# Performance work log

Hardware: AMD Instinct MI355X
Metric: run time of the kernel (lower is better)

The kernel has to match this reference:

```python
import jax, jax.numpy as jnp
import numpy as np

N = 100000   # nodes
E = 1600000  # edges
F_IN = 128
H = 128
C = 40


def setup_inputs() -> dict:
    key = jax.random.key(0)
    ks = jax.random.split(key, 8)
    s = 0.05
    return {
        "x": jax.random.normal(ks[0], (N, F_IN), dtype=jnp.float32),
        "edge_index": jax.random.randint(ks[1], (2, E), 0, N, dtype=jnp.int32),
        "W1": jax.random.normal(ks[2], (F_IN, H), dtype=jnp.float32) * s,
        "b1": jnp.zeros((H,), jnp.float32),
        "W2": jax.random.normal(ks[3], (H, H), dtype=jnp.float32) * s,
        "b2": jnp.zeros((H,), jnp.float32),
        "Wfc": jax.random.normal(ks[4], (H, C), dtype=jnp.float32) * s,
        "bfc": jnp.zeros((C,), jnp.float32),
    }


def _graph_conv(x, src, dst, norm_out, norm_in, W, b):
    # DGL GraphConv, norm='both': h = D_in^{-1/2} A D_out^{-1/2} x W + b
    h = (x * norm_out[:, None]) @ W                      # [N, H] (W first: in>=out)
    agg = jax.ops.segment_sum(h[src], dst, num_segments=N)  # gather + scatter-add
    return agg * norm_in[:, None] + b


def reference(x, edge_index, W1, b1, W2, b2, Wfc, bfc):
    src, dst = edge_index[0], edge_index[1]
    ones = jnp.ones((E,), x.dtype)
    deg_out = jnp.maximum(jax.ops.segment_sum(ones, src, num_segments=N), 1.0)
    deg_in = jnp.maximum(jax.ops.segment_sum(ones, dst, num_segments=N), 1.0)
    norm_out = jax.lax.rsqrt(deg_out)
    norm_in = jax.lax.rsqrt(deg_in)
    # layer 0: GraphConv + relu (dropout is identity in eval mode)
    h = jax.nn.relu(_graph_conv(x, src, dst, norm_out, norm_in, W1, b1))
    # layer 1: GraphConv, no activation
    h = _graph_conv(h, src, dst, norm_out, norm_in, W2, b2)
    # final FC
    return h @ Wfc + bfc
```

## Files before the change

kernel.cpp:

```cpp
#include <hip/hip_runtime.h>
#include <hip/hip_fp16.h>


#define CHUNK    4096
#define NBK      800
#define SLAB     3072

typedef __attribute__((ext_vector_type(8))) short bf16x8;
typedef __attribute__((ext_vector_type(4))) float f32x4;

struct __align__(8)  half4 { __half x, y, z, w; };
struct __align__(16) half8 { __half h[8]; };

__device__ __forceinline__ unsigned short f2bf(float f) {
    union { float f; unsigned u; } v; v.f = f;
    unsigned r = v.u + 0x7FFFu + ((v.u >> 16) & 1u);
    return (unsigned short)(r >> 16);
}
__device__ __forceinline__ float bf2f(unsigned short h) {
    union { unsigned u; float f; } v; v.u = ((unsigned)h) << 16;
    return v.f;
}

__global__ void setup_kernel(const float* __restrict__ W1, const float* __restrict__ W2,
                             const float* __restrict__ Wfc,
                             const float* __restrict__ b2, const float* __restrict__ bfc,
                             unsigned short* __restrict__ Wh1, unsigned short* __restrict__ Wl1,
                             unsigned short* __restrict__ Wh2, unsigned short* __restrict__ Wl2,
                             float* __restrict__ b2p,
                             int* __restrict__ cur_d, int* __restrict__ cur_s, int nbuck) {
    int idx = blockIdx.x * blockDim.x + threadIdx.x;
    if (idx < nbuck) { cur_d[idx] = idx * SLAB; cur_s[idx] = idx * SLAB; }

    if (idx < 16384) {
        int k = idx >> 7, nn = idx & 127;
        float v = W1[idx];
        int q = k >> 5, j = k & 7, lb = ((k >> 3) & 3) * 16;
        int tcol = nn >> 4;
        int l = lb + (nn & 15);
        int pos = ((tcol * 4 + q) * 64 + l) * 8 + j;
        unsigned short h = f2bf(v);
        Wh1[pos] = h;
        Wl1[pos] = f2bf(v - bf2f(h));
    } else if (idx < 16384 + 6144) {
        int i2 = idx - 16384;
        int k = i2 / 48, nn = i2 - k * 48;
        float v = 0.f;
        if (nn < 40) {
            const float* w2row = W2 + k * 128;
            #pragma unroll 8
            for (int jj = 0; jj < 128; ++jj) v += w2row[jj] * Wfc[jj * 40 + nn];
        }
        int t = nn >> 4, q = k >> 5, j = k & 7;
        int l = ((k >> 3) & 3) * 16 + (nn & 15);
        int pos = ((t * 4 + q) * 64 + l) * 8 + j;
        unsigned short h = f2bf(v);
        Wh2[pos] = h;
        Wl2[pos] = f2bf(v - bf2f(h));
    } else if (idx < 16384 + 6144 + 40) {
        int c = idx - (16384 + 6144);
        float a = bfc[c];
        #pragma unroll 8
        for (int j = 0; j < 128; ++j) a += b2[j] * Wfc[j * 40 + c];
        b2p[c] = a;
    }
}

__global__ __launch_bounds__(256) void scatter_res_kernel(
        const int* __restrict__ src, const int* __restrict__ dst,
        int* __restrict__ cur_d, int* __restrict__ cur_s,
        unsigned int* __restrict__ ppack, unsigned char* __restrict__ es_loc,
        int E) {
    __shared__ int hd[NBK], hs[NBK], bd[NBK], bs[NBK];
    const int tid = threadIdx.x;
    for (int i = tid; i < NBK; i += 256) { hd[i] = 0; hs[i] = 0; }
    __syncthreads();
    const int base = blockIdx.x * CHUNK;
    const int end  = min(base + CHUNK, E);
    for (int e = base + tid; e < end; e += 256) {
        atomicAdd(&hd[((unsigned)dst[e]) >> 7], 1);
        atomicAdd(&hs[((unsigned)src[e]) >> 7], 1);
    }
    __syncthreads();
    for (int i = tid; i < NBK; i += 256) {
        int cd = hd[i];
        bd[i] = cd ? atomicAdd(&cur_d[i], cd) : 0;
        hd[i] = 0;
        int cs = hs[i];
        bs[i] = cs ? atomicAdd(&cur_s[i], cs) : 0;
        hs[i] = 0;
    }
    __syncthreads();
    for (int e = base + tid; e < end; e += 256) {
        int d = dst[e], s = src[e];
        unsigned bin_d = ((unsigned)d) >> 7;
        int pos = bd[bin_d] + atomicAdd(&hd[bin_d], 1);
        ppack[pos] = (((unsigned)d & 127u) << 17) | (unsigned)s;
        unsigned bin_s = ((unsigned)s) >> 7;
        int ps = bs[bin_s] + atomicAdd(&hs[bin_s], 1);
        es_loc[ps] = (unsigned char)(s & 127);
    }
}

__global__ __launch_bounds__(256) void fine_kernel(
        const unsigned int* __restrict__ ppack, const int* __restrict__ cur_d,
        const unsigned char* __restrict__ es_loc, const int* __restrict__ cur_s,
        int* __restrict__ deg_in, float* __restrict__ norm_in,
        int* __restrict__ row_ptr, int* __restrict__ csr_src,
        float* __restrict__ norm_out, int N_) {
    __shared__ int h[128];
    __shared__ int psum[128];
    const int tid = threadIdx.x;
    const int b = blockIdx.x;
    const int start = b * SLAB;
    const int node  = (b << 7) + tid;

    const int end_d = cur_d[b];
    if (tid < 128) h[tid] = 0;
    __syncthreads();
    for (int i = start + tid; i < end_d; i += 256)
        atomicAdd(&h[ppack[i] >> 17], 1);
    __syncthreads();

    int a = 0;
    if (tid < 128) { a = h[tid]; psum[tid] = a; }
    __syncthreads();
    for (int off = 1; off < 128; off <<= 1) {
        int t = 0;
        if (tid < 128 && tid >= off) t = psum[tid - off];
        __syncthreads();
        if (tid < 128) psum[tid] += t;
        __syncthreads();
    }

    if (tid < 128) {
        int base0 = psum[tid] - a + start;
        if (node < N_) {
            deg_in[node]  = a;
            row_ptr[node] = base0;
            norm_in[node] = rsqrtf((float)(a < 1 ? 1 : a));
        }
        h[tid] = base0;
    }
    __syncthreads();

    for (int i = start + tid; i < end_d; i += 256) {
        unsigned int pk = ppack[i];
        int pos = atomicAdd(&h[pk >> 17], 1);
        csr_src[pos] = (int)(pk & 0x1FFFFu);
    }
    __syncthreads();

    const int end_s = cur_s[b];
    if (tid < 128) h[tid] = 0;
    __syncthreads();
    for (int i = start + tid; i < end_s; i += 256)
        atomicAdd(&h[(int)es_loc[i]], 1);
    __syncthreads();

    if (tid < 128 && node < N_) {
        int d = h[tid];
        norm_out[node] = rsqrtf((float)(d < 1 ? 1 : d));
    }
}

__global__ __launch_bounds__(256, 3) void gemm128(
        const float* __restrict__ X, const float* __restrict__ scale,
        const unsigned short* __restrict__ Wh, const unsigned short* __restrict__ Wl,
        __half* __restrict__ Y, int nrows) {
    const int tid  = threadIdx.x;
    const int lane = tid & 63;
    const int w    = tid >> 6;
    const int m    = lane & 15;
    const int quad = lane >> 4;
    const int rowBase = blockIdx.x * 128 + w * 32;

    bf16x8 Ah[2][4], Al[2][4];
    #pragma unroll
    for (int rt = 0; rt < 2; ++rt) {
        int r = rowBase + rt * 16 + m;
        float sc = (r < nrows) ? scale[r] : 0.f;
        const float* xr = X + (size_t)(r < nrows ? r : 0) * 128;
        #pragma unroll
        for (int q = 0; q < 4; ++q) {
            int k0 = q * 32 + quad * 8;
            float4 a = *(const float4*)(xr + k0);
            float4 bv = *(const float4*)(xr + k0 + 4);
            float v[8] = {a.x * sc, a.y * sc, a.z * sc, a.w * sc,
                          bv.x * sc, bv.y * sc, bv.z * sc, bv.w * sc};
            bf16x8 hi, lo;
            #pragma unroll
            for (int j = 0; j < 8; ++j) {
                unsigned short h = f2bf(v[j]);
                hi[j] = (short)h;
                lo[j] = (short)f2bf(v[j] - bf2f(h));
            }
            Ah[rt][q] = hi; Al[rt][q] = lo;
        }
    }

    f32x4 acc[2][8];
    #pragma unroll
    for (int rt = 0; rt < 2; ++rt)
        #pragma unroll
        for (int t = 0; t < 8; ++t)
            acc[rt][t] = (f32x4){0.f, 0.f, 0.f, 0.f};

    #pragma unroll
    for (int t = 0; t < 8; ++t) {
        #pragma unroll
        for (int q = 0; q < 4; ++q) {
            const int off = ((t * 4 + q) * 64 + lane) * 8;
            bf16x8 Bh = *(const bf16x8*)(Wh + off);
            bf16x8 Bl = *(const bf16x8*)(Wl + off);
            #pragma unroll
            for (int rt = 0; rt < 2; ++rt) {
                acc[rt][t] = __builtin_amdgcn_mfma_f32_16x16x32_bf16(Ah[rt][q], Bh, acc[rt][t], 0, 0, 0);
                acc[rt][t] = __builtin_amdgcn_mfma_f32_16x16x32_bf16(Ah[rt][q], Bl, acc[rt][t], 0, 0, 0);
                acc[rt][t] = __builtin_amdgcn_mfma_f32_16x16x32_bf16(Al[rt][q], Bh, acc[rt][t], 0, 0, 0);
            }
        }
    }

    #pragma unroll
    for (int rt = 0; rt < 2; ++rt) {
        int r0 = rowBase + rt * 16 + quad * 4;
        #pragma unroll
        for (int reg = 0; reg < 4; ++reg) {
            int r = r0 + reg;
            if (r >= nrows) continue;
            __half* yr = Y + (size_t)r * 128 + m;
            #pragma unroll
            for (int t = 0; t < 8; ++t)
                yr[t * 16] = __float2half(acc[rt][t][reg]);
        }
    }
}

__global__ __launch_bounds__(256, 4) void gather_kernel(
        const __half* __restrict__ H, const int* __restrict__ row_ptr,
        const int* __restrict__ deg, const int* __restrict__ csr_src,
        const float* __restrict__ norm_in, const float* __restrict__ b,
        const float* __restrict__ norm_out,
        const unsigned short* __restrict__ Wh2, const unsigned short* __restrict__ Wl2,
        __half* __restrict__ G, int n) {
    __shared__ unsigned short h1h[16][136];
    __shared__ unsigned short h1l[16][136];
    const int tid   = threadIdx.x;
    const int node0 = blockIdx.x * 16;
    const int g     = tid >> 4;
    const int node  = node0 + g;
    const int c     = (tid & 15) * 8;
    const bool active = node < n;

    int start = 0, cnt = 0;
    if (active) { start = row_ptr[node]; cnt = deg[node]; }
    float acc[8] = {0.f, 0.f, 0.f, 0.f, 0.f, 0.f, 0.f, 0.f};

    int j = 0;
    for (; j + 4 <= cnt; j += 4) {
        int s0 = csr_src[start + j];
        int s1 = csr_src[start + j + 1];
        int s2 = csr_src[start + j + 2];
        int s3 = csr_src[start + j + 3];
        half8 v0 = *(const half8*)(H + (long long)s0 * 128 + c);
        half8 v1 = *(const half8*)(H + (long long)s1 * 128 + c);
        half8 v2 = *(const half8*)(H + (long long)s2 * 128 + c);
        half8 v3 = *(const half8*)(H + (long long)s3 * 128 + c);
        #pragma unroll
        for (int k = 0; k < 8; ++k)
            acc[k] += (__half2float(v0.h[k]) + __half2float(v1.h[k]))
                    + (__half2float(v2.h[k]) + __half2float(v3.h[k]));
    }
    for (; j < cnt; ++j) {
        int s0 = csr_src[start + j];
        half8 v0 = *(const half8*)(H + (long long)s0 * 128 + c);
        #pragma unroll
        for (int k = 0; k < 8; ++k) acc[k] += __half2float(v0.h[k]);
    }

    float ni = active ? norm_in[node]  : 0.f;
    float no = active ? norm_out[node] : 0.f;
    float4 b0  = *(const float4*)(b + c);
    float4 b1v = *(const float4*)(b + c + 4);
    float bb[8] = {b0.x, b0.y, b0.z, b0.w, b1v.x, b1v.y, b1v.z, b1v.w};
    bf16x8 hi, lo;
    #pragma unroll
    for (int k = 0; k < 8; ++k) {
        float hv = fmaxf(acc[k] * ni + bb[k], 0.f) * no;
        unsigned short h = f2bf(hv);
        hi[k] = (short)h;
        lo[k] = (short)f2bf(hv - bf2f(h));
    }
    *(bf16x8*)&h1h[g][c] = hi;
    *(bf16x8*)&h1l[g][c] = lo;
    __syncthreads();

    const int w = tid >> 6;
    if (w < 3) {
        const int lane = tid & 63;
        const int m    = lane & 15;
        const int quad = lane >> 4;

        f32x4 a3 = (f32x4){0.f, 0.f, 0.f, 0.f};
        const int t = w;
        #pragma unroll
        for (int q = 0; q < 4; ++q) {
            const int k0 = q * 32 + quad * 8;
            bf16x8 Ah = *(const bf16x8*)&h1h[m][k0];
            bf16x8 Al = *(const bf16x8*)&h1l[m][k0];
            const int off = ((t * 4 + q) * 64 + lane) * 8;
            bf16x8 Bh = *(const bf16x8*)(Wh2 + off);
            bf16x8 Bl = *(const bf16x8*)(Wl2 + off);
            a3 = __builtin_amdgcn_mfma_f32_16x16x32_bf16(Ah, Bh, a3, 0, 0, 0);
            a3 = __builtin_amdgcn_mfma_f32_16x16x32_bf16(Ah, Bl, a3, 0, 0, 0);
            a3 = __builtin_amdgcn_mfma_f32_16x16x32_bf16(Al, Bh, a3, 0, 0, 0);
        }

        const int col = t * 16 + m;
        if (col < 40) {
            const int r0 = node0 + quad * 4;
            #pragma unroll
            for (int reg = 0; reg < 4; ++reg) {
                int r = r0 + reg;
                if (r < n) G[(size_t)r * 64 + col] = __float2half(a3[reg]);
            }
        }
    }
}

__global__ __launch_bounds__(256) void gather40_kernel(
        const __half* __restrict__ G, const int* __restrict__ row_ptr,
        const int* __restrict__ deg, const int* __restrict__ csr_src,
        const float* __restrict__ norm_in, const float* __restrict__ b2p,
        float* __restrict__ out, int n) {
    const int t = blockIdx.x * 256 + threadIdx.x;
    if (t >= n * 5) return;
    const int node = t / 5;
    const int c    = (t - node * 5) * 8;

    const int start = row_ptr[node];
    const int cnt   = deg[node];
    float acc[8] = {0.f, 0.f, 0.f, 0.f, 0.f, 0.f, 0.f, 0.f};

    int j = 0;
    for (; j + 4 <= cnt; j += 4) {
        int s0 = csr_src[start + j];
        int s1 = csr_src[start + j + 1];
        int s2 = csr_src[start + j + 2];
        int s3 = csr_src[start + j + 3];
        half8 v0 = *(const half8*)(G + (long long)s0 * 64 + c);
        half8 v1 = *(const half8*)(G + (long long)s1 * 64 + c);
        half8 v2 = *(const half8*)(G + (long long)s2 * 64 + c);
        half8 v3 = *(const half8*)(G + (long long)s3 * 64 + c);
        #pragma unroll
        for (int k = 0; k < 8; ++k)
            acc[k] += (__half2float(v0.h[k]) + __half2float(v1.h[k]))
                    + (__half2float(v2.h[k]) + __half2float(v3.h[k]));
    }
    for (; j < cnt; ++j) {
        int s0 = csr_src[start + j];
        half8 v0 = *(const half8*)(G + (long long)s0 * 64 + c);
        #pragma unroll
        for (int k = 0; k < 8; ++k) acc[k] += __half2float(v0.h[k]);
    }

    float ni = norm_in[node];
    float4 o0, o1;
    o0.x = acc[0] * ni + b2p[c + 0];
    o0.y = acc[1] * ni + b2p[c + 1];
    o0.z = acc[2] * ni + b2p[c + 2];
    o0.w = acc[3] * ni + b2p[c + 3];
    o1.x = acc[4] * ni + b2p[c + 4];
    o1.y = acc[5] * ni + b2p[c + 5];
    o1.z = acc[6] * ni + b2p[c + 6];
    o1.w = acc[7] * ni + b2p[c + 7];
    float* op = out + (long long)node * 40 + c;
    *(float4*)(op)     = o0;
    *(float4*)(op + 4) = o1;
}

extern "C" void kernel_launch(void* const* d_in, const int* in_sizes, int n_in,
                              void* d_out, int out_size, void* d_ws, size_t ws_size,
                              hipStream_t stream) {
    const float* x   = (const float*)d_in[0];
    const int*   ei  = (const int*)  d_in[1];
    const float* W1  = (const float*)d_in[2];
    const float* b1  = (const float*)d_in[3];
    const float* W2  = (const float*)d_in[4];
    const float* b2  = (const float*)d_in[5];
    const float* Wfc = (const float*)d_in[6];
    const float* bfc = (const float*)d_in[7];
    float* out = (float*)d_out;

    const int N = in_sizes[0] / 128;
    const int E = in_sizes[1] / 2;
    const int* src = ei;
    const int* dst = ei + E;

    const int nbuck = (N + 127) >> 7;
    const int B1 = (E + CHUNK - 1) / CHUNK;

    char* p = (char*)d_ws;
    float* norm_out = (float*)p; p += (size_t)N * 4;
    float* norm_in  = (float*)p; p += (size_t)N * 4;
    float* bufA     = (float*)p; p += (size_t)N * 128 * 4;
    float* bufB     = (float*)p; p += (size_t)N * 128 * 4;
    int*   deg_in   = (int*)p;   p += (size_t)N * 4;
    int*   row_ptr  = (int*)p;   p += (size_t)N * 4;
    int*   csr_src  = (int*)p;   p += (size_t)NBK * SLAB * 4;
    int*   cur_d    = (int*)p;   p += (size_t)1024 * 4;
    int*   cur_s    = (int*)p;   p += (size_t)1024 * 4;
    float* b2p      = (float*)p; p += (size_t)64 * 4;
    unsigned short* Wh1 = (unsigned short*)p; p += (size_t)16384 * 2;
    unsigned short* Wl1 = (unsigned short*)p; p += (size_t)16384 * 2;
    unsigned short* Wh2 = (unsigned short*)p; p += (size_t)6144 * 2;
    unsigned short* Wl2 = (unsigned short*)p; p += (size_t)6144 * 2;

    unsigned int*  ppack  = (unsigned int*)bufB;
    unsigned char* es_loc = (unsigned char*)(ppack + (size_t)NBK * SLAB);

    __half* h1pre = (__half*)bufA;
    __half* G     = (__half*)bufB;

    const int T = 256;

    setup_kernel<<<(16384 + 6144 + 40 + T - 1) / T, T, 0, stream>>>(
        W1, W2, Wfc, b2, bfc, Wh1, Wl1, Wh2, Wl2, b2p, cur_d, cur_s, nbuck);
    scatter_res_kernel<<<B1, T, 0, stream>>>(src, dst, cur_d, cur_s, ppack, es_loc, E);
    fine_kernel<<<nbuck, T, 0, stream>>>(ppack, cur_d, es_loc, cur_s,
                                         deg_in, norm_in, row_ptr, csr_src,
                                         norm_out, N);

    const int gemm_grid = (N + 127) / 128;
    gemm128<<<gemm_grid, T, 0, stream>>>(x, norm_out, Wh1, Wl1, h1pre, N);
    const int gather_grid = (N + 15) / 16;
    gather_kernel<<<gather_grid, T, 0, stream>>>(h1pre, row_ptr, deg_in, csr_src,
                                                 norm_in, b1, norm_out,
                                                 Wh2, Wl2, G, N);
    gather40_kernel<<<((size_t)N * 5 + T - 1) / T, T, 0, stream>>>(
        G, row_ptr, deg_in, csr_src, norm_in, b2p, out, N);
}
```

Before: 277.5 us.

## Fuse edge scatter with layer-1 GEMM and move norm_out into gather

The layer-1 GEMM no longer scales rows by norm_out, so it no longer depends on the degree computation. It is merged into the edge-scatter launch as extra blocks, letting the two independent stages run at the same time and removing one kernel launch. To make up for it, the gather kernel loads norm_out for every source edge and multiplies it in with fma. This adds 1.6M scattered 4-byte reads in exchange for the overlap, and the fused kernel now shares LDS and register limits between two very different workloads.

New measurement: 276.6 us. No clear change (-0.3%).

```diff
diff --git a/kernel.cpp b/kernel.cpp
--- a/kernel.cpp
+++ b/kernel.cpp
@@ -66,39 +66,114 @@
     }
 }
 
-__global__ __launch_bounds__(256) void scatter_res_kernel(
+__global__ __launch_bounds__(256, 3) void fat_kernel(
         const int* __restrict__ src, const int* __restrict__ dst,
         int* __restrict__ cur_d, int* __restrict__ cur_s,
         unsigned int* __restrict__ ppack, unsigned char* __restrict__ es_loc,
-        int E) {
+        int E, int nsc,
+        const float* __restrict__ X,
+        const unsigned short* __restrict__ Wh, const unsigned short* __restrict__ Wl,
+        __half* __restrict__ Y, int nrows) {
     __shared__ int hd[NBK], hs[NBK], bd[NBK], bs[NBK];
     const int tid = threadIdx.x;
-    for (int i = tid; i < NBK; i += 256) { hd[i] = 0; hs[i] = 0; }
-    __syncthreads();
-    const int base = blockIdx.x * CHUNK;
-    const int end  = min(base + CHUNK, E);
-    for (int e = base + tid; e < end; e += 256) {
-        atomicAdd(&hd[((unsigned)dst[e]) >> 7], 1);
-        atomicAdd(&hs[((unsigned)src[e]) >> 7], 1);
-    }
-    __syncthreads();
-    for (int i = tid; i < NBK; i += 256) {
-        int cd = hd[i];
-        bd[i] = cd ? atomicAdd(&cur_d[i], cd) : 0;
-        hd[i] = 0;
-        int cs = hs[i];
-        bs[i] = cs ? atomicAdd(&cur_s[i], cs) : 0;
-        hs[i] = 0;
-    }
-    __syncthreads();
-    for (int e = base + tid; e < end; e += 256) {
-        int d = dst[e], s = src[e];
-        unsigned bin_d = ((unsigned)d) >> 7;
-        int pos = bd[bin_d] + atomicAdd(&hd[bin_d], 1);
-        ppack[pos] = (((unsigned)d & 127u) << 17) | (unsigned)s;
-        unsigned bin_s = ((unsigned)s) >> 7;
-        int ps = bs[bin_s] + atomicAdd(&hs[bin_s], 1);
-        es_loc[ps] = (unsigned char)(s & 127);
+
+    if (blockIdx.x < nsc) {
+        for (int i = tid; i < NBK; i += 256) { hd[i] = 0; hs[i] = 0; }
+        __syncthreads();
+        const int base = blockIdx.x * CHUNK;
+        const int end  = min(base + CHUNK, E);
+        for (int e = base + tid; e < end; e += 256) {
+            atomicAdd(&hd[((unsigned)dst[e]) >> 7], 1);
+            atomicAdd(&hs[((unsigned)src[e]) >> 7], 1);
+        }
+        __syncthreads();
+        for (int i = tid; i < NBK; i += 256) {
+            int cd = hd[i];
+            bd[i] = cd ? atomicAdd(&cur_d[i], cd) : 0;
+            hd[i] = 0;
+            int cs = hs[i];
+            bs[i] = cs ? atomicAdd(&cur_s[i], cs) : 0;
+            hs[i] = 0;
+        }
+        __syncthreads();
+        for (int e = base + tid; e < end; e += 256) {
+            int d = dst[e], s = src[e];
+            unsigned bin_d = ((unsigned)d) >> 7;
+            int pos = bd[bin_d] + atomicAdd(&hd[bin_d], 1);
+            ppack[pos] = (((unsigned)d & 127u) << 17) | (unsigned)s;
+            unsigned bin_s = ((unsigned)s) >> 7;
+            int ps = bs[bin_s] + atomicAdd(&hs[bin_s], 1);
+            es_loc[ps] = (unsigned char)(s & 127);
+        }
+        return;
+    }
+
+    const int blk  = blockIdx.x - nsc;
+    const int lane = tid & 63;
+    const int w    = tid >> 6;
+    const int m    = lane & 15;
+    const int quad = lane >> 4;
+    const int rowBase = blk * 128 + w * 32;
+
+    bf16x8 Ah[2][4], Al[2][4];
+    #pragma unroll
+    for (int rt = 0; rt < 2; ++rt) {
+        int r = rowBase + rt * 16 + m;
+        const float* xr = X + (size_t)(r < nrows ? r : 0) * 128;
+        const float z = (r < nrows) ? 1.f : 0.f;
+        #pragma unroll
+        for (int q = 0; q < 4; ++q) {
+            int k0 = q * 32 + quad * 8;
+            float4 a = *(const float4*)(xr + k0);
+            float4 bv = *(const float4*)(xr + k0 + 4);
+            float v[8] = {a.x * z, a.y * z, a.z * z, a.w * z,
+                          bv.x * z, bv.y * z, bv.z * z, bv.w * z};
+            bf16x8 hi, lo;
+            #pragma unroll
+            for (int j = 0; j < 8; ++j) {
+                unsigned short h = f2bf(v[j]);
+                hi[j] = (short)h;
+                lo[j] = (short)f2bf(v[j] - bf2f(h));
+            }
+            Ah[rt][q] = hi; Al[rt][q] = lo;
+        }
+    }
+
+    f32x4 acc[2][8];
+    #pragma unroll
+    for (int rt = 0; rt < 2; ++rt)
+        #pragma unroll
+        for (int t = 0; t < 8; ++t)
+            acc[rt][t] = (f32x4){0.f, 0.f, 0.f, 0.f};
+
+    #pragma unroll
+    for (int t = 0; t < 8; ++t) {
+        #pragma unroll
+        for (int q = 0; q < 4; ++q) {
+            const int off = ((t * 4 + q) * 64 + lane) * 8;
+            bf16x8 Bh = *(const bf16x8*)(Wh + off);
+            bf16x8 Bl = *(const bf16x8*)(Wl + off);
+            #pragma unroll
+            for (int rt = 0; rt < 2; ++rt) {
+                acc[rt][t] = __builtin_amdgcn_mfma_f32_16x16x32_bf16(Ah[rt][q], Bh, acc[rt][t], 0, 0, 0);
+                acc[rt][t] = __builtin_amdgcn_mfma_f32_16x16x32_bf16(Ah[rt][q], Bl, acc[rt][t], 0, 0, 0);
+                acc[rt][t] = __builtin_amdgcn_mfma_f32_16x16x32_bf16(Al[rt][q], Bh, acc[rt][t], 0, 0, 0);
+            }
+        }
+    }
+
+    #pragma unroll
+    for (int rt = 0; rt < 2; ++rt) {
+        int r0 = rowBase + rt * 16 + quad * 4;
+        #pragma unroll
+        for (int reg = 0; reg < 4; ++reg) {
+            int r = r0 + reg;
+            if (r >= nrows) continue;
+            __half* yr = Y + (size_t)r * 128 + m;
+            #pragma unroll
+            for (int t = 0; t < 8; ++t)
+                yr[t * 16] = __float2half(acc[rt][t][reg]);
+        }
     }
 }
 
@@ -161,79 +236,6 @@
     if (tid < 128 && node < N_) {
         int d = h[tid];
         norm_out[node] = rsqrtf((float)(d < 1 ? 1 : d));
-    }
-}
-
-__global__ __launch_bounds__(256, 3) void gemm128(
-        const float* __restrict__ X, const float* __restrict__ scale,
-        const unsigned short* __restrict__ Wh, const unsigned short* __restrict__ Wl,
-        __half* __restrict__ Y, int nrows) {
-    const int tid  = threadIdx.x;
-    const int lane = tid & 63;
-    const int w    = tid >> 6;
-    const int m    = lane & 15;
-    const int quad = lane >> 4;
-    const int rowBase = blockIdx.x * 128 + w * 32;
-
-    bf16x8 Ah[2][4], Al[2][4];
-    #pragma unroll
-    for (int rt = 0; rt < 2; ++rt) {
-        int r = rowBase + rt * 16 + m;
-        float sc = (r < nrows) ? scale[r] : 0.f;
-        const float* xr = X + (size_t)(r < nrows ? r : 0) * 128;
-        #pragma unroll
-        for (int q = 0; q < 4; ++q) {
-            int k0 = q * 32 + quad * 8;
-            float4 a = *(const float4*)(xr + k0);
-            float4 bv = *(const float4*)(xr + k0 + 4);
-            float v[8] = {a.x * sc, a.y * sc, a.z * sc, a.w * sc,
-                          bv.x * sc, bv.y * sc, bv.z * sc, bv.w * sc};
-            bf16x8 hi, lo;
-            #pragma unroll
-            for (int j = 0; j < 8; ++j) {
-                unsigned short h = f2bf(v[j]);
-                hi[j] = (short)h;
-                lo[j] = (short)f2bf(v[j] - bf2f(h));
-            }
-            Ah[rt][q] = hi; Al[rt][q] = lo;
-        }
-    }
-
-    f32x4 acc[2][8];
-    #pragma unroll
-    for (int rt = 0; rt < 2; ++rt)
-        #pragma unroll
-        for (int t = 0; t < 8; ++t)
-            acc[rt][t] = (f32x4){0.f, 0.f, 0.f, 0.f};
-
-    #pragma unroll
-    for (int t = 0; t < 8; ++t) {
-        #pragma unroll
-        for (int q = 0; q < 4; ++q) {
-            const int off = ((t * 4 + q) * 64 + lane) * 8;
-            bf16x8 Bh = *(const bf16x8*)(Wh + off);
-            bf16x8 Bl = *(const bf16x8*)(Wl + off);
-            #pragma unroll
-            for (int rt = 0; rt < 2; ++rt) {
-                acc[rt][t] = __builtin_amdgcn_mfma_f32_16x16x32_bf16(Ah[rt][q], Bh, acc[rt][t], 0, 0, 0);
-                acc[rt][t] = __builtin_amdgcn_mfma_f32_16x16x32_bf16(Ah[rt][q], Bl, acc[rt][t], 0, 0, 0);
-                acc[rt][t] = __builtin_amdgcn_mfma_f32_16x16x32_bf16(Al[rt][q], Bh, acc[rt][t], 0, 0, 0);
-            }
-        }
-    }
-
-    #pragma unroll
-    for (int rt = 0; rt < 2; ++rt) {
-        int r0 = rowBase + rt * 16 + quad * 4;
-        #pragma unroll
-        for (int reg = 0; reg < 4; ++reg) {
-            int r = r0 + reg;
-            if (r >= nrows) continue;
-            __half* yr = Y + (size_t)r * 128 + m;
-            #pragma unroll
-            for (int t = 0; t < 8; ++t)
-                yr[t * 16] = __float2half(acc[rt][t][reg]);
-        }
     }
 }
 
@@ -263,20 +265,24 @@
         int s1 = csr_src[start + j + 1];
         int s2 = csr_src[start + j + 2];
         int s3 = csr_src[start + j + 3];
+        float n0 = norm_out[s0], n1 = norm_out[s1];
+        float n2 = norm_out[s2], n3 = norm_out[s3];
         half8 v0 = *(const half8*)(H + (long long)s0 * 128 + c);
         half8 v1 = *(const half8*)(H + (long long)s1 * 128 + c);
         half8 v2 = *(const half8*)(H + (long long)s2 * 128 + c);
         half8 v3 = *(const half8*)(H + (long long)s3 * 128 + c);
         #pragma unroll
-        for (int k = 0; k < 8; ++k)
-            acc[k] += (__half2float(v0.h[k]) + __half2float(v1.h[k]))
-                    + (__half2float(v2.h[k]) + __half2float(v3.h[k]));
+        for (int k = 0; k < 8; ++k) {
+            float t0 = fmaf(n0, __half2float(v0.h[k]), fmaf(n1, __half2float(v1.h[k]), acc[k]));
+            acc[k] = fmaf(n2, __half2float(v2.h[k]), fmaf(n3, __half2float(v3.h[k]), t0));
+        }
     }
     for (; j < cnt; ++j) {
         int s0 = csr_src[start + j];
+        float n0 = norm_out[s0];
         half8 v0 = *(const half8*)(H + (long long)s0 * 128 + c);
         #pragma unroll
-        for (int k = 0; k < 8; ++k) acc[k] += __half2float(v0.h[k]);
+        for (int k = 0; k < 8; ++k) acc[k] = fmaf(n0, __half2float(v0.h[k]), acc[k]);
     }
 
     float ni = active ? norm_in[node]  : 0.f;
@@ -399,7 +405,8 @@
     const int* dst = ei + E;
 
     const int nbuck = (N + 127) >> 7;
-    const int B1 = (E + CHUNK - 1) / CHUNK;
+    const int nsc   = (E + CHUNK - 1) / CHUNK;
+    const int gemm_grid = (N + 127) / 128;
 
     char* p = (char*)d_ws;
     float* norm_out = (float*)p; p += (size_t)N * 4;
@@ -427,13 +434,12 @@
 
     setup_kernel<<<(16384 + 6144 + 40 + T - 1) / T, T, 0, stream>>>(
         W1, W2, Wfc, b2, bfc, Wh1, Wl1, Wh2, Wl2, b2p, cur_d, cur_s, nbuck);
-    scatter_res_kernel<<<B1, T, 0, stream>>>(src, dst, cur_d, cur_s, ppack, es_loc, E);
+    fat_kernel<<<nsc + gemm_grid, T, 0, stream>>>(
+        src, dst, cur_d, cur_s, ppack, es_loc, E, nsc,
+        x, Wh1, Wl1, h1pre, N);
     fine_kernel<<<nbuck, T, 0, stream>>>(ppack, cur_d, es_loc, cur_s,
                                          deg_in, norm_in, row_ptr, csr_src,
                                          norm_out, N);
-
-    const int gemm_grid = (N + 127) / 128;
-    gemm128<<<gemm_grid, T, 0, stream>>>(x, norm_out, Wh1, Wl1, h1pre, N);
     const int gather_grid = (N + 15) / 16;
     gather_kernel<<<gather_grid, T, 0, stream>>>(h1pre, row_ptr, deg_in, csr_src,
                                                  norm_in, b1, norm_out,
```
